# Kernel tuning notes

Hardware: AMD Instinct MI355X
Metric: run time of the kernel (lower is better)

## Reference

```python
import jax, jax.numpy as jnp
import numpy as np

N_NODES = 100000
N_EDGES = 3200000
IN_DIM, HID_DIM, OUT_DIM = 256, 64, 32


def setup_inputs() -> dict:
    key = jax.random.key(0)
    ks = jax.random.split(key, 12)
    s = 0.05
    x = jax.random.normal(ks[0], (N_NODES, IN_DIM), dtype=jnp.float32)
    edge_index = jax.random.randint(ks[1], (2, N_EDGES), 0, N_NODES, dtype=jnp.int64)
    return {
        "x": x,
        "edge_index": edge_index,
        # GCNConv 1: in->hid
        "W1": jax.random.normal(ks[2], (IN_DIM, HID_DIM), dtype=jnp.float32) * s,
        "b1": jnp.zeros((HID_DIM,), dtype=jnp.float32),
        # GCNConv 2: hid->out
        "W2": jax.random.normal(ks[3], (HID_DIM, OUT_DIM), dtype=jnp.float32) * s,
        "b2": jnp.zeros((OUT_DIM,), dtype=jnp.float32),
        # weight_predictor MLP: Linear(out,hid) -> ReLU -> Linear(hid,1) -> Sigmoid
        "Wp1": jax.random.normal(ks[4], (OUT_DIM, HID_DIM), dtype=jnp.float32) * s,
        "bp1": jnp.zeros((HID_DIM,), dtype=jnp.float32),
        "Wp2": jax.random.normal(ks[5], (HID_DIM, 1), dtype=jnp.float32) * s,
        "bp2": jnp.zeros((1,), dtype=jnp.float32),
    }


def gcn_conv(h, src, dst, deg_norm, W, b, n_nodes):
    """PyG GCNConv: x' = D^-1/2 (A+I) D^-1/2 (x W) + b, edges incl. self-loops."""
    h = h @ W                                   # [N, F_out]
    coef = deg_norm[src] * deg_norm[dst]        # [E+N]
    agg = jax.ops.segment_sum(h[src] * coef[:, None], dst, num_segments=n_nodes)
    return agg + b


def reference(x, edge_index, W1, b1, W2, b2, Wp1, bp1, Wp2, bp2):
    n = x.shape[0]
    loop = jnp.arange(n, dtype=edge_index.dtype)
    src = jnp.concatenate([edge_index[0], loop])  # self-loops appended
    dst = jnp.concatenate([edge_index[1], loop])
    # degree (with self-loops) on target nodes, deg^-1/2 with inf->0
    deg = jax.ops.segment_sum(jnp.ones_like(dst, dtype=x.dtype), dst, num_segments=n)
    deg_norm = jnp.where(deg > 0, jax.lax.rsqrt(deg), 0.0)

    h = gcn_conv(x, src, dst, deg_norm, W1, b1, n)
    h = jax.nn.relu(h)                            # dropout inactive (eval)
    h = gcn_conv(h, src, dst, deg_norm, W2, b2, n)  # no relu after last conv

    # weight predictor MLP head
    p = jax.nn.relu(h @ Wp1 + bp1)
    node_weights = jax.nn.sigmoid(p @ Wp2 + bp2)  # [N, 1]
    return h, node_weights
```

## Files before the change

### kernel.cpp

```cpp
#include <hip/hip_runtime.h>
#include <hip/hip_fp16.h>
#include <cstdint>
#include <cstddef>

#define N_NODES 100000
#define N_EDGES 3200000
#define IN_DIM  256
#define HID_DIM 64
#define OUT_DIM 32

#define NBINS      391
#define BIN_SHIFT  8
#define BIN_STRIDE 9216
#define BIN_EPB    8192

typedef unsigned int uint;
typedef unsigned char uchar;
typedef unsigned short ushort;

__device__ __forceinline__ float2 h2tof2(uint u) {
    __half2 h = *reinterpret_cast<const __half2*>(&u);
    return __half22float2(h);
}
__device__ __forceinline__ uint f2toh2(float a, float b) {
    __half2 h = __floats2half2_rn(a, b);
    return *reinterpret_cast<const uint*>(&h);
}
__device__ __forceinline__ ushort f2h(float a) {
    __half h = __float2half_rn(a);
    return *reinterpret_cast<const ushort*>(&h);
}

__global__ __launch_bounds__(512)
void k_bin(const int* __restrict__ ei, int* __restrict__ bin_cursor,
           uint* __restrict__ binned, int* __restrict__ bin_base,
           int* __restrict__ rowptr) {
    __shared__ int   lcount[NBINS];
    __shared__ int   lstart[NBINS];
    __shared__ int   lplace[NBINS];
    __shared__ int   gbase[NBINS];
    __shared__ int   sc[512];
    __shared__ uint  stage[BIN_EPB];
    __shared__ uchar binid[BIN_EPB];

    const int tid  = threadIdx.x;
    const int bid  = blockIdx.x;
    int*      done = bin_cursor + NBINS;

    const int e0   = bid * BIN_EPB;
    const int nval = min(BIN_EPB, N_EDGES - e0);

    for (int i = tid; i < NBINS; i += 512) lcount[i] = 0;
    __syncthreads();

    #pragma unroll
    for (int k = 0; k < BIN_EPB / 512; ++k) {
        int e = e0 + k * 512 + tid;
        if (e < N_EDGES) atomicAdd(&lcount[ei[N_EDGES + e] >> BIN_SHIFT], 1);
    }
    __syncthreads();

    int v = (tid < NBINS) ? lcount[tid] : 0;
    sc[tid] = v; __syncthreads();
    for (int off = 1; off < 512; off <<= 1) {
        int x = sc[tid];
        if (tid >= off) x += sc[tid - off];
        __syncthreads(); sc[tid] = x; __syncthreads();
    }
    if (tid < NBINS) {
        int excl = sc[tid] - v;
        lstart[tid] = excl;
        lplace[tid] = excl;
        gbase[tid]  = atomicAdd(&bin_cursor[tid], v);
    }
    __syncthreads();

    #pragma unroll
    for (int k = 0; k < BIN_EPB / 512; ++k) {
        int e = e0 + k * 512 + tid;
        if (e < N_EDGES) {
            int s = ei[e];
            int d = ei[N_EDGES + e];
            int b = d >> BIN_SHIFT;
            int p = atomicAdd(&lplace[b], 1);
            stage[p] = (uint)s | ((uint)(d & 255) << 17) | ((uint)(b >> 8) << 25);
            binid[p] = (uchar)(b & 255);
        }
    }
    __syncthreads();

    for (int i = tid; i < nval; i += 512) {
        uint ed = stage[i];
        int  b  = (int)binid[i] | (int)((ed >> 25) & 1u) << 8;
        int  gix = gbase[b] + (i - lstart[b]);
        if (gix < BIN_STRIDE)
            binned[(size_t)b * BIN_STRIDE + gix] = ed;
    }
    __syncthreads();

    if (tid == 0) {
        __threadfence();
        lcount[0] = (atomicAdd(done, 1) == gridDim.x - 1) ? 1 : 0;
    }
    __syncthreads();
    if (lcount[0]) {
        int t = tid;
        int vv = 0;
        if (t < NBINS) vv = min(atomicAdd(&bin_cursor[t], 0), BIN_STRIDE);
        sc[t] = vv; __syncthreads();
        for (int off = 1; off < 512; off <<= 1) {
            int x = sc[t];
            if (t >= off) x += sc[t - off];
            __syncthreads(); sc[t] = x; __syncthreads();
        }
        if (t < NBINS)      bin_base[t] = sc[t] - vv;
        if (t == NBINS - 1) rowptr[N_NODES] = sc[t];
    }
}

template<int KD, int NC>
__global__ __launch_bounds__(32 * (NC / 8))
void k_gemm_h(const float* __restrict__ X, const float* __restrict__ W,
              uint* __restrict__ Yh, int M) {
    constexpr int TC = NC / 8;
    constexpr int THREADS = 32 * TC;
    constexpr int KC = 32;
    __shared__ float Xs[128][33];
    __shared__ float Ws[KC][NC];

    const int tid  = threadIdx.x;
    const int tr   = tid / TC;
    const int tc   = tid % TC;
    const int row0 = blockIdx.x * 128;

    float acc[4][8];
    #pragma unroll
    for (int i = 0; i < 4; ++i)
        #pragma unroll
        for (int j = 0; j < 8; ++j) acc[i][j] = 0.f;

    for (int kc = 0; kc < KD; kc += KC) {
        #pragma unroll
        for (int i = tid; i < 128 * (KC / 4); i += THREADS) {
            int r  = i / (KC / 4);
            int k4 = (i % (KC / 4)) * 4;
            float4 v = make_float4(0.f, 0.f, 0.f, 0.f);
            int gr = row0 + r;
            if (gr < M)
                v = *reinterpret_cast<const float4*>(&X[(size_t)gr * KD + kc + k4]);
            Xs[r][k4 + 0] = v.x; Xs[r][k4 + 1] = v.y;
            Xs[r][k4 + 2] = v.z; Xs[r][k4 + 3] = v.w;
        }
        #pragma unroll
        for (int i = tid; i < KC * (NC / 4); i += THREADS) {
            int kk = i / (NC / 4);
            int c4 = (i % (NC / 4)) * 4;
            *reinterpret_cast<float4*>(&Ws[kk][c4]) =
                *reinterpret_cast<const float4*>(&W[(size_t)(kc + kk) * NC + c4]);
        }
        __syncthreads();

        #pragma unroll
        for (int kk = 0; kk < KC; ++kk) {
            float xv[4];
            #pragma unroll
            for (int i = 0; i < 4; ++i) xv[i] = Xs[tr * 4 + i][kk];
            float4 w0 = *reinterpret_cast<const float4*>(&Ws[kk][tc * 8]);
            float4 w1 = *reinterpret_cast<const float4*>(&Ws[kk][tc * 8 + 4]);
            float wv[8] = {w0.x, w0.y, w0.z, w0.w, w1.x, w1.y, w1.z, w1.w};
            #pragma unroll
            for (int i = 0; i < 4; ++i)
                #pragma unroll
                for (int j = 0; j < 8; ++j)
                    acc[i][j] = fmaf(xv[i], wv[j], acc[i][j]);
        }
        __syncthreads();
    }

    #pragma unroll
    for (int i = 0; i < 4; ++i) {
        int gr = row0 + tr * 4 + i;
        if (gr < M) {
            uint4 o;
            o.x = f2toh2(acc[i][0], acc[i][1]);
            o.y = f2toh2(acc[i][2], acc[i][3]);
            o.z = f2toh2(acc[i][4], acc[i][5]);
            o.w = f2toh2(acc[i][6], acc[i][7]);
            *reinterpret_cast<uint4*>(&Yh[(size_t)gr * (NC / 2) + tc * 4]) = o;
        }
    }
}

__global__ __launch_bounds__(256)
void k_csr(const uint* __restrict__ binned, const int* __restrict__ bin_cursor,
           const int* __restrict__ bin_base, int* __restrict__ rowptr,
           float* __restrict__ dn, int* __restrict__ csr) {
    __shared__ int lcnt[256];
    __shared__ int lpl[256];
    __shared__ int sc[256];
    __shared__ int csr_s[BIN_STRIDE];

    const int tid   = threadIdx.x;
    const int b     = blockIdx.x;
    const int n0    = b << BIN_SHIFT;
    const int cnt   = min(bin_cursor[b], BIN_STRIDE);
    const int ebase = bin_base[b];
    const uint* bb  = binned + (size_t)b * BIN_STRIDE;

    lcnt[tid] = 0;
    __syncthreads();
    for (int i = tid; i < cnt; i += 256)
        atomicAdd(&lcnt[(bb[i] >> 17) & 255u], 1);
    __syncthreads();

    int v = lcnt[tid];
    sc[tid] = v; __syncthreads();
    for (int off = 1; off < 256; off <<= 1) {
        int x = sc[tid];
        if (tid >= off) x += sc[tid - off];
        __syncthreads(); sc[tid] = x; __syncthreads();
    }
    int excl = sc[tid] - v;
    lpl[tid] = excl;
    int n = n0 + tid;
    if (n < N_NODES) {
        rowptr[n] = ebase + excl;
        dn[n]     = rsqrtf((float)v + 1.0f);
    }
    __syncthreads();

    for (int i = tid; i < cnt; i += 256) {
        uint ed = bb[i];
        int  p  = atomicAdd(&lpl[(ed >> 17) & 255u], 1);
        csr_s[p] = (int)(ed & 0x1FFFFu);
    }
    __syncthreads();
    for (int i = tid; i < cnt; i += 256)
        csr[ebase + i] = csr_s[i];
}

__global__ __launch_bounds__(256)
void k_agg1(const uint* __restrict__ H1h, const int* __restrict__ rowptr,
            const int* __restrict__ csr, const float* __restrict__ dn,
            const float* __restrict__ b1, const float* __restrict__ W2,
            ushort* __restrict__ H2h) {
    __shared__ float W2s[HID_DIM * OUT_DIM];
    for (int i = threadIdx.x; i < HID_DIM * OUT_DIM; i += 256) W2s[i] = W2[i];
    __syncthreads();

    int wid  = (blockIdx.x * blockDim.x + threadIdx.x) >> 6;
    int lane = threadIdx.x & 63;
    if (wid >= N_NODES / 2) return;
    const int half = lane >> 5;
    const int hb   = half << 5;
    const int l    = lane & 31;
    const int n    = 2 * wid + half;

    int rp = (l < 2) ? rowptr[n + l] : 0;
    int base = __shfl(rp, hb + 0);
    int cnt  = __shfl(rp, hb + 1) - base;
    const float dnn = dn[n];

    float2 self2 = h2tof2(H1h[(size_t)n * 32 + l]);
    float2 acc;
    acc.x = dnn * self2.x;
    acc.y = dnn * self2.y;

    const int cnt2 = max(cnt, __shfl_xor(cnt, 32));
    for (int b0 = 0; b0 < cnt2; b0 += 32) {
        int m_own = min(32, cnt - b0);
        int m_max = min(32, cnt2 - b0);
        int s = 0; float dsv = 0.f;
        if (l < m_own) { s = csr[base + b0 + l]; dsv = dn[s]; }
        for (int j0 = 0; j0 < m_max; j0 += 8) {
            uint v[8]; float w[8];
            #pragma unroll
            for (int i = 0; i < 8; ++i) {
                int j  = j0 + i;
                int sj = __shfl(s, hb + j);
                w[i] = __shfl(dsv, hb + j);
                v[i] = H1h[(size_t)sj * 32 + l];
            }
            #pragma unroll
            for (int i = 0; i < 8; ++i) {
                float2 vf = h2tof2(v[i]);
                acc.x = fmaf(w[i], vf.x, acc.x);
                acc.y = fmaf(w[i], vf.y, acc.y);
            }
        }
    }
    float2 b1q = *reinterpret_cast<const float2*>(b1 + 2 * l);
    float2 o;
    o.x = fmaxf(b1q.x + dnn * acc.x, 0.f);
    o.y = fmaxf(b1q.y + dnn * acc.y, 0.f);

    const int c = lane & 31, hh = lane >> 5;
    #pragma unroll
    for (int nodesel = 0; nodesel < 2; ++nodesel) {
        const int nb = nodesel << 5;
        float acc2 = 0.f;
        #pragma unroll
        for (int fi = 0; fi < 32; ++fi) {
            int f = hh * 32 + fi;
            float vv = (f & 1) ? __shfl(o.y, nb + (f >> 1))
                               : __shfl(o.x, nb + (f >> 1));
            acc2 = fmaf(vv, W2s[f * OUT_DIM + c], acc2);
        }
        acc2 += __shfl_xor(acc2, 32);
        if (hh == 0) H2h[(size_t)(2 * wid + nodesel) * 32 + c] = f2h(acc2);
    }
}

__global__ __launch_bounds__(256)
void k_agg2m(const uint* __restrict__ H2h, const int* __restrict__ rowptr,
             const int* __restrict__ csr, const float* __restrict__ dn,
             const float* __restrict__ b2, const float* __restrict__ Wp1,
             const float* __restrict__ bp1, const float* __restrict__ Wp2,
             const float* __restrict__ bp2, float* __restrict__ out_h,
             float* __restrict__ out_w) {
    __shared__ float Wp1s[OUT_DIM * HID_DIM];
    __shared__ float Wp2s[HID_DIM];
    __shared__ float bp1s[HID_DIM];
    for (int i = threadIdx.x; i < OUT_DIM * HID_DIM; i += 256) Wp1s[i] = Wp1[i];
    if (threadIdx.x < HID_DIM) {
        Wp2s[threadIdx.x] = Wp2[threadIdx.x];
        bp1s[threadIdx.x] = bp1[threadIdx.x];
    }
    __syncthreads();

    int wid  = (blockIdx.x * blockDim.x + threadIdx.x) >> 6;
    int lane = threadIdx.x & 63;
    if (wid >= N_NODES / 2) return;
    const int nd  = lane >> 5;
    const int nb0 = nd << 5;
    const int l32 = lane & 31;
    const int l   = lane & 15;
    const int h2  = (lane >> 4) & 1;
    const int n   = 2 * wid + nd;

    int rp = (lane < 3) ? rowptr[2 * wid + lane] : 0;
    int base = __shfl(rp, nd);
    int cnt  = __shfl(rp, nd + 1) - base;
    const float dnn = dn[n];

    float2 self2 = h2tof2(H2h[(size_t)n * 16 + l]);
    float2 acc;
    acc.x = (h2 == 0) ? dnn * self2.x : 0.f;
    acc.y = (h2 == 0) ? dnn * self2.y : 0.f;

    const int cnt2 = max(cnt, __shfl_xor(cnt, 32));
    for (int b0 = 0; b0 < cnt2; b0 += 32) {
        int m_own = min(32, cnt - b0);
        int m_max = min(32, cnt2 - b0);
        int s = 0; float dsv = 0.f;
        if (l32 < m_own) { s = csr[base + b0 + l32]; dsv = dn[s]; }
        for (int j0 = h2; j0 < m_max; j0 += 16) {
            uint v[8]; float w[8];
            #pragma unroll
            for (int i = 0; i < 8; ++i) {
                int j  = j0 + 2 * i;
                int sj = __shfl(s, nb0 + j);
                w[i] = __shfl(dsv, nb0 + j);
                v[i] = H2h[(size_t)sj * 16 + l];
            }
            #pragma unroll
            for (int i = 0; i < 8; ++i) {
                float2 vf = h2tof2(v[i]);
                acc.x = fmaf(w[i], vf.x, acc.x);
                acc.y = fmaf(w[i], vf.y, acc.y);
            }
        }
    }
    acc.x += __shfl_xor(acc.x, 16);
    acc.y += __shfl_xor(acc.y, 16);
    float2 b2q = *reinterpret_cast<const float2*>(b2 + 2 * l);
    float2 hv;
    hv.x = b2q.x + dnn * acc.x;
    hv.y = b2q.y + dnn * acc.y;
    if (h2 == 0)
        *reinterpret_cast<float2*>(out_h + (size_t)n * OUT_DIM + 2 * l) = hv;

    #pragma unroll
    for (int nodesel = 0; nodesel < 2; ++nodesel) {
        const int nb = nodesel << 5;
        float p = bp1s[lane];
        #pragma unroll
        for (int ff = 0; ff < OUT_DIM; ++ff) {
            float hf = (ff & 1) ? __shfl(hv.y, nb + (ff >> 1))
                                : __shfl(hv.x, nb + (ff >> 1));
            p = fmaf(hf, Wp1s[ff * HID_DIM + lane], p);
        }
        p = fmaxf(p, 0.f);
        float z = p * Wp2s[lane];
        #pragma unroll
        for (int off = 32; off; off >>= 1) z += __shfl_xor(z, off);
        if (lane == 0)
            out_w[2 * wid + nodesel] = 1.f / (1.f + __expf(-(z + bp2[0])));
    }
}

extern "C" void kernel_launch(void* const* d_in, const int* in_sizes, int n_in,
                              void* d_out, int out_size, void* d_ws, size_t ws_size,
                              hipStream_t stream) {
    const float* x   = (const float*)d_in[0];
    const int*   ei  = (const int*)d_in[1];
    const float* W1  = (const float*)d_in[2];
    const float* b1  = (const float*)d_in[3];
    const float* W2  = (const float*)d_in[4];
    const float* b2  = (const float*)d_in[5];
    const float* Wp1 = (const float*)d_in[6];
    const float* bp1 = (const float*)d_in[7];
    const float* Wp2 = (const float*)d_in[8];
    const float* bp2 = (const float*)d_in[9];
    float* out = (float*)d_out;

    char* ws = (char*)d_ws;
    int*    bin_cursor = (int*)   (ws + 0);
    int*    bin_base   = (int*)   (ws + 2048);
    int*    rowptr     = (int*)   (ws + 4096);
    float*  dn         = (float*) (ws + 404480);
    int*    csr        = (int*)   (ws + 804608);
    uint*   binned     = (uint*)  (ws + 13604608);
    uint*   H1h        = (uint*)  (ws + 28018432);
    ushort* H2h        = (ushort*)(ws + 40818432);

    hipMemsetAsync(bin_cursor, 0, (NBINS + 1) * sizeof(int), stream);

    k_bin<<<(N_EDGES + BIN_EPB - 1) / BIN_EPB, 512, 0, stream>>>(ei, bin_cursor, binned,
                                                                 bin_base, rowptr);
    k_gemm_h<IN_DIM, HID_DIM><<<(N_NODES + 127) / 128, 256, 0, stream>>>(x, W1, H1h, N_NODES);
    k_csr<<<NBINS, 256, 0, stream>>>(binned, bin_cursor, bin_base, rowptr, dn, csr);

    k_agg1<<<(N_NODES / 2 + 3) / 4, 256, 0, stream>>>(H1h, rowptr, csr, dn, b1, W2, H2h);
    k_agg2m<<<(N_NODES / 2 + 3) / 4, 256, 0, stream>>>((const uint*)H2h, rowptr, csr, dn, b2,
                                                       Wp1, bp1, Wp2, bp2,
                                                       out, out + (size_t)N_NODES * OUT_DIM);
}
```

Before: 295.0 us.

## Merge CSR build and GEMM into one launch; use fma_mix in aggregation

Merges the independent CSR-construction kernel and the X·W1 GEMM kernel into one grid, with block ranges dispatching to either role and sharing a unioned shared-memory buffer. This drops one kernel launch and lets the two workloads run concurrently on the GPU. The aggregation inner loops also switch from half-to-float conversion plus fmaf to inline-asm v_fma_mix_f32, which reads the fp16 halves directly and removes the conversion instructions. The cost is that the merged kernel's shared-memory footprint is the larger of the two roles, which may limit occupancy for the GEMM blocks.

```diff
diff --git a/kernel.cpp b/kernel.cpp
--- a/kernel.cpp
+++ b/kernel.cpp
@@ -29,6 +29,14 @@
 __device__ __forceinline__ ushort f2h(float a) {
     __half h = __float2half_rn(a);
     return *reinterpret_cast<const ushort*>(&h);
+}
+__device__ __forceinline__ void fma_mix_lo(float& acc, float w, uint v) {
+    asm("v_fma_mix_f32 %0, %1, %2, %0 op_sel:[0,0,0] op_sel_hi:[0,1,0]"
+        : "+v"(acc) : "v"(w), "v"(v));
+}
+__device__ __forceinline__ void fma_mix_hi(float& acc, float w, uint v) {
+    asm("v_fma_mix_f32 %0, %1, %2, %0 op_sel:[0,1,0] op_sel_hi:[0,1,0]"
+        : "+v"(acc) : "v"(w), "v"(v));
 }
 
 __global__ __launch_bounds__(512)
@@ -118,125 +126,126 @@
     }
 }
 
-template<int KD, int NC>
-__global__ __launch_bounds__(32 * (NC / 8))
-void k_gemm_h(const float* __restrict__ X, const float* __restrict__ W,
-              uint* __restrict__ Yh, int M) {
-    constexpr int TC = NC / 8;
-    constexpr int THREADS = 32 * TC;
-    constexpr int KC = 32;
-    __shared__ float Xs[128][33];
-    __shared__ float Ws[KC][NC];
-
-    const int tid  = threadIdx.x;
-    const int tr   = tid / TC;
-    const int tc   = tid % TC;
-    const int row0 = blockIdx.x * 128;
-
-    float acc[4][8];
-    #pragma unroll
-    for (int i = 0; i < 4; ++i)
+#define SMEM2_BYTES 39936
+
+__global__ __launch_bounds__(256)
+void k_csr_gemm(const uint* __restrict__ binned, const int* __restrict__ bin_cursor,
+                const int* __restrict__ bin_base, int* __restrict__ rowptr,
+                float* __restrict__ dn, int* __restrict__ csr,
+                const float* __restrict__ X, const float* __restrict__ W,
+                uint* __restrict__ Yh) {
+    __shared__ __align__(16) char smem[SMEM2_BYTES];
+    const int tid = threadIdx.x;
+    const int bid = blockIdx.x;
+
+    if (bid < NBINS) {
+        int* lcnt  = (int*)(smem);
+        int* lpl   = (int*)(smem + 1024);
+        int* sc    = (int*)(smem + 2048);
+        int* csr_s = (int*)(smem + 3072);
+
+        const int b     = bid;
+        const int n0    = b << BIN_SHIFT;
+        const int cnt   = min(bin_cursor[b], BIN_STRIDE);
+        const int ebase = bin_base[b];
+        const uint* bb  = binned + (size_t)b * BIN_STRIDE;
+
+        lcnt[tid] = 0;
+        __syncthreads();
+        for (int i = tid; i < cnt; i += 256)
+            atomicAdd(&lcnt[(bb[i] >> 17) & 255u], 1);
+        __syncthreads();
+
+        int v = lcnt[tid];
+        sc[tid] = v; __syncthreads();
+        for (int off = 1; off < 256; off <<= 1) {
+            int x = sc[tid];
+            if (tid >= off) x += sc[tid - off];
+            __syncthreads(); sc[tid] = x; __syncthreads();
+        }
+        int excl = sc[tid] - v;
+        lpl[tid] = excl;
+        int n = n0 + tid;
+        if (n < N_NODES) {
+            rowptr[n] = ebase + excl;
+            dn[n]     = rsqrtf((float)v + 1.0f);
+        }
+        __syncthreads();
+
+        for (int i = tid; i < cnt; i += 256) {
+            uint ed = bb[i];
+            int  p  = atomicAdd(&lpl[(ed >> 17) & 255u], 1);
+            csr_s[p] = (int)(ed & 0x1FFFFu);
+        }
+        __syncthreads();
+        for (int i = tid; i < cnt; i += 256)
+            csr[ebase + i] = csr_s[i];
+    } else {
+        constexpr int KD = IN_DIM, NC = HID_DIM, KC = 32;
+        float* Xs = (float*)(smem);
+        float* Ws = (float*)(smem + 16896);
+        const int tr   = tid / 8;
+        const int tc   = tid % 8;
+        const int row0 = (bid - NBINS) * 128;
+        const int M    = N_NODES;
+
+        float acc[4][8];
         #pragma unroll
-        for (int j = 0; j < 8; ++j) acc[i][j] = 0.f;
-
-    for (int kc = 0; kc < KD; kc += KC) {
+        for (int i = 0; i < 4; ++i)
+            #pragma unroll
+            for (int j = 0; j < 8; ++j) acc[i][j] = 0.f;
+
+        for (int kc = 0; kc < KD; kc += KC) {
+            #pragma unroll
+            for (int i = tid; i < 128 * (KC / 4); i += 256) {
+                int r  = i / (KC / 4);
+                int k4 = (i % (KC / 4)) * 4;
+                float4 vv = make_float4(0.f, 0.f, 0.f, 0.f);
+                int gr = row0 + r;
+                if (gr < M)
+                    vv = *reinterpret_cast<const float4*>(&X[(size_t)gr * KD + kc + k4]);
+                Xs[r * 33 + k4 + 0] = vv.x; Xs[r * 33 + k4 + 1] = vv.y;
+                Xs[r * 33 + k4 + 2] = vv.z; Xs[r * 33 + k4 + 3] = vv.w;
+            }
+            #pragma unroll
+            for (int i = tid; i < KC * (NC / 4); i += 256) {
+                int kk = i / (NC / 4);
+                int c4 = (i % (NC / 4)) * 4;
+                *reinterpret_cast<float4*>(&Ws[kk * NC + c4]) =
+                    *reinterpret_cast<const float4*>(&W[(size_t)(kc + kk) * NC + c4]);
+            }
+            __syncthreads();
+
+            #pragma unroll
+            for (int kk = 0; kk < KC; ++kk) {
+                float xv[4];
+                #pragma unroll
+                for (int i = 0; i < 4; ++i) xv[i] = Xs[(tr * 4 + i) * 33 + kk];
+                float4 w0 = *reinterpret_cast<const float4*>(&Ws[kk * NC + tc * 8]);
+                float4 w1 = *reinterpret_cast<const float4*>(&Ws[kk * NC + tc * 8 + 4]);
+                float wv[8] = {w0.x, w0.y, w0.z, w0.w, w1.x, w1.y, w1.z, w1.w};
+                #pragma unroll
+                for (int i = 0; i < 4; ++i)
+                    #pragma unroll
+                    for (int j = 0; j < 8; ++j)
+                        acc[i][j] = fmaf(xv[i], wv[j], acc[i][j]);
+            }
+            __syncthreads();
+        }
+
         #pragma unroll
-        for (int i = tid; i < 128 * (KC / 4); i += THREADS) {
-            int r  = i / (KC / 4);
-            int k4 = (i % (KC / 4)) * 4;
-            float4 v = make_float4(0.f, 0.f, 0.f, 0.f);
-            int gr = row0 + r;
-            if (gr < M)
-                v = *reinterpret_cast<const float4*>(&X[(size_t)gr * KD + kc + k4]);
-            Xs[r][k4 + 0] = v.x; Xs[r][k4 + 1] = v.y;
-            Xs[r][k4 + 2] = v.z; Xs[r][k4 + 3] = v.w;
-        }
-        #pragma unroll
-        for (int i = tid; i < KC * (NC / 4); i += THREADS) {
-            int kk = i / (NC / 4);
-            int c4 = (i % (NC / 4)) * 4;
-            *reinterpret_cast<float4*>(&Ws[kk][c4]) =
-                *reinterpret_cast<const float4*>(&W[(size_t)(kc + kk) * NC + c4]);
-        }
-        __syncthreads();
-
-        #pragma unroll
-        for (int kk = 0; kk < KC; ++kk) {
-            float xv[4];
-            #pragma unroll
-            for (int i = 0; i < 4; ++i) xv[i] = Xs[tr * 4 + i][kk];
-            float4 w0 = *reinterpret_cast<const float4*>(&Ws[kk][tc * 8]);
-            float4 w1 = *reinterpret_cast<const float4*>(&Ws[kk][tc * 8 + 4]);
-            float wv[8] = {w0.x, w0.y, w0.z, w0.w, w1.x, w1.y, w1.z, w1.w};
-            #pragma unroll
-            for (int i = 0; i < 4; ++i)
-                #pragma unroll
-                for (int j = 0; j < 8; ++j)
-                    acc[i][j] = fmaf(xv[i], wv[j], acc[i][j]);
-        }
-        __syncthreads();
-    }
-
-    #pragma unroll
-    for (int i = 0; i < 4; ++i) {
-        int gr = row0 + tr * 4 + i;
-        if (gr < M) {
-            uint4 o;
-            o.x = f2toh2(acc[i][0], acc[i][1]);
-            o.y = f2toh2(acc[i][2], acc[i][3]);
-            o.z = f2toh2(acc[i][4], acc[i][5]);
-            o.w = f2toh2(acc[i][6], acc[i][7]);
-            *reinterpret_cast<uint4*>(&Yh[(size_t)gr * (NC / 2) + tc * 4]) = o;
-        }
-    }
-}
-
-__global__ __launch_bounds__(256)
-void k_csr(const uint* __restrict__ binned, const int* __restrict__ bin_cursor,
-           const int* __restrict__ bin_base, int* __restrict__ rowptr,
-           float* __restrict__ dn, int* __restrict__ csr) {
-    __shared__ int lcnt[256];
-    __shared__ int lpl[256];
-    __shared__ int sc[256];
-    __shared__ int csr_s[BIN_STRIDE];
-
-    const int tid   = threadIdx.x;
-    const int b     = blockIdx.x;
-    const int n0    = b << BIN_SHIFT;
-    const int cnt   = min(bin_cursor[b], BIN_STRIDE);
-    const int ebase = bin_base[b];
-    const uint* bb  = binned + (size_t)b * BIN_STRIDE;
-
-    lcnt[tid] = 0;
-    __syncthreads();
-    for (int i = tid; i < cnt; i += 256)
-        atomicAdd(&lcnt[(bb[i] >> 17) & 255u], 1);
-    __syncthreads();
-
-    int v = lcnt[tid];
-    sc[tid] = v; __syncthreads();
-    for (int off = 1; off < 256; off <<= 1) {
-        int x = sc[tid];
-        if (tid >= off) x += sc[tid - off];
-        __syncthreads(); sc[tid] = x; __syncthreads();
-    }
-    int excl = sc[tid] - v;
-    lpl[tid] = excl;
-    int n = n0 + tid;
-    if (n < N_NODES) {
-        rowptr[n] = ebase + excl;
-        dn[n]     = rsqrtf((float)v + 1.0f);
-    }
-    __syncthreads();
-
-    for (int i = tid; i < cnt; i += 256) {
-        uint ed = bb[i];
-        int  p  = atomicAdd(&lpl[(ed >> 17) & 255u], 1);
-        csr_s[p] = (int)(ed & 0x1FFFFu);
-    }
-    __syncthreads();
-    for (int i = tid; i < cnt; i += 256)
-        csr[ebase + i] = csr_s[i];
+        for (int i = 0; i < 4; ++i) {
+            int gr = row0 + tr * 4 + i;
+            if (gr < M) {
+                uint4 o;
+                o.x = f2toh2(acc[i][0], acc[i][1]);
+                o.y = f2toh2(acc[i][2], acc[i][3]);
+                o.z = f2toh2(acc[i][4], acc[i][5]);
+                o.w = f2toh2(acc[i][6], acc[i][7]);
+                *reinterpret_cast<uint4*>(&Yh[(size_t)gr * (NC / 2) + tc * 4]) = o;
+            }
+        }
+    }
 }
 
 __global__ __launch_bounds__(256)
@@ -283,9 +292,8 @@
             }
             #pragma unroll
             for (int i = 0; i < 8; ++i) {
-                float2 vf = h2tof2(v[i]);
-                acc.x = fmaf(w[i], vf.x, acc.x);
-                acc.y = fmaf(w[i], vf.y, acc.y);
+                fma_mix_lo(acc.x, w[i], v[i]);
+                fma_mix_hi(acc.y, w[i], v[i]);
             }
         }
     }
@@ -365,9 +373,8 @@
             }
             #pragma unroll
             for (int i = 0; i < 8; ++i) {
-                float2 vf = h2tof2(v[i]);
-                acc.x = fmaf(w[i], vf.x, acc.x);
-                acc.y = fmaf(w[i], vf.y, acc.y);
+                fma_mix_lo(acc.x, w[i], v[i]);
+                fma_mix_hi(acc.y, w[i], v[i]);
             }
         }
     }
@@ -428,8 +435,8 @@
 
     k_bin<<<(N_EDGES + BIN_EPB - 1) / BIN_EPB, 512, 0, stream>>>(ei, bin_cursor, binned,
                                                                  bin_base, rowptr);
-    k_gemm_h<IN_DIM, HID_DIM><<<(N_NODES + 127) / 128, 256, 0, stream>>>(x, W1, H1h, N_NODES);
-    k_csr<<<NBINS, 256, 0, stream>>>(binned, bin_cursor, bin_base, rowptr, dn, csr);
+    k_csr_gemm<<<NBINS + (N_NODES + 127) / 128, 256, 0, stream>>>(
+        binned, bin_cursor, bin_base, rowptr, dn, csr, x, W1, H1h);
 
     k_agg1<<<(N_NODES / 2 + 3) / 4, 256, 0, stream>>>(H1h, rowptr, csr, dn, b1, W2, H2h);
     k_agg2m<<<(N_NODES / 2 + 3) / 4, 256, 0, stream>>>((const uint*)H2h, rowptr, csr, dn, b2,
```

Measured after the change: 287.4 us. 1.03x faster.
